# Optimization experiments

Hardware: AMD Instinct MI355X
Metric: run time of the kernel (lower is better)

## Reference

```python
import jax, jax.numpy as jnp
import numpy as np

IMAGE_SIZE = 512


def setup_inputs() -> dict:
    key = jax.random.key(0)
    k1, k2, k3, k4, k5 = jax.random.split(key, 5)
    B, S, C, P = 64, IMAGE_SIZE, 64, IMAGE_SIZE * IMAGE_SIZE
    x = jax.random.normal(k1, (B, S, S), dtype=jnp.float32)
    pattern_importance = jax.random.uniform(k2, (B, C), dtype=jnp.float32)
    idxx = jax.random.randint(k3, (P,), 0, S)
    idxy = jax.random.randint(k4, (P,), 0, S)
    cluster_id = jax.random.randint(k5, (P,), 0, C)
    return {"x": x, "pattern_importance": pattern_importance,
            "idxx": idxx, "idxy": idxy, "cluster_id": cluster_id}


def reference(x, pattern_importance, idxx, idxy, cluster_id):
    S = IMAGE_SIZE
    # fft2 with zero-pad/crop to (S, S), then shift DC to center
    x_fft = jnp.fft.fftshift(jnp.fft.fft2(x, s=(S, S), axes=(-2, -1)), axes=(-2, -1))
    # mask: ones everywhere, per-cluster importance scattered at clustered freq bins
    B = x.shape[0]
    mask = jnp.ones((B, S, S), dtype=x.dtype)
    # mask[j, idxx, idxy] = pattern_importance[j, cluster_id] for all batches j at once
    mask = mask.at[:, idxx, idxy].set(pattern_importance[:, cluster_id])
    x_reject = x_fft * mask
    x_ifft = jnp.real(jnp.fft.ifft2(jnp.fft.ifftshift(x_reject, axes=(-2, -1)),
                                    s=(x.shape[1], x.shape[2]), axes=(-2, -1)))
    return x_ifft
```

## Files before the change

kernel.cpp:

```cpp
#include <hip/hip_runtime.h>

#define INV_N2 (1.0f/262144.0f)
#define RS 264
#define TS 520
#define YH_F2 ((size_t)32768 * RS)

typedef unsigned u32x2 __attribute__((ext_vector_type(2)));

__device__ __forceinline__ int brev9(int v) { return (int)(__brev((unsigned)v) >> 23); }

__device__ __forceinline__ float hsin(float rev) { return __builtin_amdgcn_sinf(rev); }
__device__ __forceinline__ float hcos(float rev) { return __builtin_amdgcn_cosf(rev); }

template<int CTRL>
__device__ __forceinline__ float xdpp(float x) {
  int v = __float_as_int(x);
  return __int_as_float(__builtin_amdgcn_update_dpp(v, v, CTRL, 0xF, 0xF, true));
}
__device__ __forceinline__ float xs1(float x) { return xdpp<0xB1>(x); }
__device__ __forceinline__ float xs2(float x) { return xdpp<0x4E>(x); }
__device__ __forceinline__ float xs8(float x) { return xdpp<0x128>(x); }
__device__ __forceinline__ float xs4(float x) {
  return __int_as_float(__builtin_amdgcn_ds_swizzle(__float_as_int(x), 0x101F));
}
__device__ __forceinline__ float xs16(float x) {
#if __has_builtin(__builtin_amdgcn_permlane16_swap)
  u32x2 r = __builtin_amdgcn_permlane16_swap(__float_as_uint(x), __float_as_uint(x), false, false);
  return __uint_as_float((threadIdx.x & 16) ? r[0] : r[1]);
#else
  return __int_as_float(__builtin_amdgcn_ds_swizzle(__float_as_int(x), 0x401F));
#endif
}
__device__ __forceinline__ float xs32(float x) {
#if __has_builtin(__builtin_amdgcn_permlane32_swap)
  u32x2 r = __builtin_amdgcn_permlane32_swap(__float_as_uint(x), __float_as_uint(x), false, false);
  return __uint_as_float((threadIdx.x & 32) ? r[0] : r[1]);
#else
  return __shfl_xor(x, 32, 64);
#endif
}

__device__ __forceinline__ void bfly_dif(float &ar, float &ai, float &br, float &bi,
                                         float wr, float wi) {
  float sr = ar + br, si = ai + bi;
  float dr = ar - br, di = ai - bi;
  ar = sr; ai = si;
  br = dr*wr - di*wi; bi = dr*wi + di*wr;
}
__device__ __forceinline__ void bfly_dit(float &ar, float &ai, float &br, float &bi,
                                         float wr, float wi) {
  float tr = br*wr - bi*wi, ti = br*wi + bi*wr;
  br = ar - tr; bi = ai - ti;
  ar = ar + tr; ai = ai + ti;
}

#define FWD_XSTAGE(S, XCHG) { \
  const float rev = -(float)(lane & (S-1)) * (0.5f/(float)(S)); \
  float s0 = hsin(rev), c0 = hcos(rev); \
  const bool up = (lane & (S)) != 0; \
  const float sg = up ? -1.0f : 1.0f; \
  const float wr = up ? c0 : 1.0f; \
  const float wi = up ? s0 : 0.0f; \
  _Pragma("unroll") for (int k = 0; k < 8; ++k) { \
    float rr = XCHG(xr[k]); float ri = XCHG(xi[k]); \
    float vr = fmaf(sg, xr[k], rr); float vi = fmaf(sg, xi[k], ri); \
    xr[k] = vr*wr - vi*wi; xi[k] = vr*wi + vi*wr; } }

#define INV_XSTAGE(S, XCHG) { \
  const float rev = (float)(lane & (S-1)) * (0.5f/(float)(S)); \
  float s0 = hsin(rev), c0 = hcos(rev); \
  const bool up = (lane & (S)) != 0; \
  const float wr = up ? c0 : 1.0f; \
  const float wi = up ? s0 : 0.0f; \
  const float sg = up ? -1.0f : 1.0f; \
  _Pragma("unroll") for (int k = 0; k < 8; ++k) { \
    float zr = xr[k]*wr - xi[k]*wi; \
    float zi = xr[k]*wi + xi[k]*wr; \
    float rr = XCHG(zr); float ri = XCHG(zi); \
    xr[k] = fmaf(sg, zr, rr); xi[k] = fmaf(sg, zi, ri); } }

__device__ __forceinline__ void wave_fft512_fwd(float xr[8], float xi[8], int lane) {
  {
    float rev = -(float)lane * (1.0f/512.0f);
    float s0 = hsin(rev), c0 = hcos(rev);
    float wr = c0, wi = s0;
    const float rr8 = 0.70710678118654752f, ri8 = -0.70710678118654752f;
    #pragma unroll
    for (int k = 0; k < 4; ++k) {
      bfly_dif(xr[k], xi[k], xr[k+4], xi[k+4], wr, wi);
      float nr = wr*rr8 - wi*ri8, ni = wr*ri8 + wi*rr8;
      wr = nr; wi = ni;
    }
  }
  {
    float rev = -(float)lane * (1.0f/256.0f);
    float s0 = hsin(rev), c0 = hcos(rev);
    float w0r = c0, w0i = s0;
    float w1r = s0, w1i = -c0;
    bfly_dif(xr[0], xi[0], xr[2], xi[2], w0r, w0i);
    bfly_dif(xr[1], xi[1], xr[3], xi[3], w1r, w1i);
    bfly_dif(xr[4], xi[4], xr[6], xi[6], w0r, w0i);
    bfly_dif(xr[5], xi[5], xr[7], xi[7], w1r, w1i);
  }
  {
    float rev = -(float)lane * (1.0f/128.0f);
    float s0 = hsin(rev), c0 = hcos(rev);
    bfly_dif(xr[0], xi[0], xr[1], xi[1], c0, s0);
    bfly_dif(xr[2], xi[2], xr[3], xi[3], c0, s0);
    bfly_dif(xr[4], xi[4], xr[5], xi[5], c0, s0);
    bfly_dif(xr[6], xi[6], xr[7], xi[7], c0, s0);
  }
  FWD_XSTAGE(32, xs32)
  FWD_XSTAGE(16, xs16)
  FWD_XSTAGE(8,  xs8)
  FWD_XSTAGE(4,  xs4)
  FWD_XSTAGE(2,  xs2)
  {
    const float sg = (lane & 1) ? -1.0f : 1.0f;
    #pragma unroll
    for (int k = 0; k < 8; ++k) {
      float rr = xs1(xr[k]); float ri = xs1(xi[k]);
      xr[k] = fmaf(sg, xr[k], rr); xi[k] = fmaf(sg, xi[k], ri);
    }
  }
}

__device__ __forceinline__ void wave_fft512_inv(float xr[8], float xi[8], int lane) {
  {
    const float sg = (lane & 1) ? -1.0f : 1.0f;
    #pragma unroll
    for (int k = 0; k < 8; ++k) {
      float rr = xs1(xr[k]); float ri = xs1(xi[k]);
      xr[k] = fmaf(sg, xr[k], rr); xi[k] = fmaf(sg, xi[k], ri);
    }
  }
  INV_XSTAGE(2,  xs2)
  INV_XSTAGE(4,  xs4)
  INV_XSTAGE(8,  xs8)
  INV_XSTAGE(16, xs16)
  INV_XSTAGE(32, xs32)
  {
    float rev = (float)lane * (1.0f/128.0f);
    float s0 = hsin(rev), c0 = hcos(rev);
    bfly_dit(xr[0], xi[0], xr[1], xi[1], c0, s0);
    bfly_dit(xr[2], xi[2], xr[3], xi[3], c0, s0);
    bfly_dit(xr[4], xi[4], xr[5], xi[5], c0, s0);
    bfly_dit(xr[6], xi[6], xr[7], xi[7], c0, s0);
  }
  {
    float rev = (float)lane * (1.0f/256.0f);
    float s0 = hsin(rev), c0 = hcos(rev);
    float w0r = c0, w0i = s0;
    float w1r = -s0, w1i = c0;
    bfly_dit(xr[0], xi[0], xr[2], xi[2], w0r, w0i);
    bfly_dit(xr[1], xi[1], xr[3], xi[3], w1r, w1i);
    bfly_dit(xr[4], xi[4], xr[6], xi[6], w0r, w0i);
    bfly_dit(xr[5], xi[5], xr[7], xi[7], w1r, w1i);
  }
  {
    float rev = (float)lane * (1.0f/512.0f);
    float s0 = hsin(rev), c0 = hcos(rev);
    float wr = c0, wi = s0;
    const float rr8 = 0.70710678118654752f, ri8 = 0.70710678118654752f;
    #pragma unroll
    for (int k = 0; k < 4; ++k) {
      bfly_dit(xr[k], xi[k], xr[k+4], xi[k+4], wr, wi);
      float nr = wr*rr8 - wi*ri8, ni = wr*ri8 + wi*rr8;
      wr = nr; wi = ni;
    }
  }
}

__global__ void k_scatter(const int* __restrict__ idxx, const int* __restrict__ idxy,
                          const int* __restrict__ cid, int* __restrict__ W) {
  int p = blockIdx.x * 256 + threadIdx.x;
  int u = (idxx[p] + 256) & 511;
  int v = (idxy[p] + 256) & 511;
  atomicMax(&W[u * 512 + v], (p << 6) | cid[p]);
}

__global__ void k_pack(const int* __restrict__ W, int* __restrict__ pk) {
  int idx = blockIdx.x * 256 + threadIdx.x;
  if (idx >= 264 * 512) return;
  int j = idx >> 9, n = idx & 511;
  int out = (127 << 7) | 127;
  if (j < 257) {
    int v = (j == 256) ? 256 : brev9(2 * j);
    int u = brev9(n);
    int c1 = W[u * 512 + v];
    int c2 = W[((512 - u) & 511) * 512 + ((512 - v) & 511)];
    int a = (c1 < 0) ? 127 : (c1 & 63);
    int b = (c2 < 0) ? 127 : (c2 & 63);
    out = (b << 7) | a;
  }
  pk[j * 512 + n] = out;
}

__global__ __launch_bounds__(512) void k_fwd_rows(const float* __restrict__ x,
                                                  float2* __restrict__ Yh) {
  int w = threadIdx.x >> 6, lane = threadIdx.x & 63;
  int r = blockIdx.x * 8 + w;
  const float* row = x + (size_t)r * 512;
  float xr[8], xi[8];
  #pragma unroll
  for (int k = 0; k < 8; ++k) { xr[k] = row[k*64 + lane]; xi[k] = 0.f; }
  wave_fft512_fwd(xr, xi, lane);
  float2* orow = Yh + (size_t)r * RS;
  if (!(lane & 1)) {
    #pragma unroll
    for (int k = 0; k < 8; ++k) orow[k*32 + (lane >> 1)] = make_float2(xr[k], xi[k]);
  } else if (lane == 1) {
    orow[256] = make_float2(xr[0], xi[0]);
  }
}

__global__ __launch_bounds__(512) void k_cols(float2* __restrict__ Yh,
                                              const int* __restrict__ pk,
                                              const float* __restrict__ pimp) {
  __shared__ float lre[8 * TS], lim[8 * TS];
  __shared__ float pilx[128];
  int tid = threadIdx.x;
  int b = blockIdx.x / 33, g = blockIdx.x % 33;
  float2* base = Yh + (size_t)b * 512 * RS + g * 8;
  #pragma unroll
  for (int rep = 0; rep < 4; ++rep) {
    int m = rep * 512 + tid;
    int i = m >> 2, cp = m & 3;
    float4 v = *(const float4*)(base + (size_t)i * RS + 2 * cp);
    lre[(2*cp)  *TS + i] = v.x; lim[(2*cp)  *TS + i] = v.y;
    lre[(2*cp+1)*TS + i] = v.z; lim[(2*cp+1)*TS + i] = v.w;
  }
  if (tid < 128) pilx[tid] = (tid < 64) ? pimp[b * 64 + tid] : 1.0f;
  __syncthreads();
  int w = tid >> 6, lane = tid & 63;
  float xr[8], xi[8];
  #pragma unroll
  for (int k = 0; k < 8; ++k) {
    xr[k] = lre[w*TS + k*64 + lane];
    xi[k] = lim[w*TS + k*64 + lane];
  }
  wave_fft512_fwd(xr, xi, lane);
  const int* cm = pk + (g * 8 + w) * 512;
  #pragma unroll
  for (int k = 0; k < 8; ++k) {
    int p = cm[k*64 + lane];
    float mm = 0.5f * (pilx[p & 127] + pilx[(p >> 7) & 127]) * INV_N2;
    xr[k] *= mm; xi[k] *= mm;
  }
  wave_fft512_inv(xr, xi, lane);
  #pragma unroll
  for (int k = 0; k < 8; ++k) {
    lre[w*TS + k*64 + lane] = xr[k];
    lim[w*TS + k*64 + lane] = xi[k];
  }
  __syncthreads();
  #pragma unroll
  for (int rep = 0; rep < 4; ++rep) {
    int m = rep * 512 + tid;
    int i = m >> 2, cp = m & 3;
    *(float4*)(base + (size_t)i * RS + 2 * cp) =
      make_float4(lre[(2*cp)*TS + i], lim[(2*cp)*TS + i],
                  lre[(2*cp+1)*TS + i], lim[(2*cp+1)*TS + i]);
  }
}

__global__ __launch_bounds__(512) void k_inv_rows(const float2* __restrict__ Yh,
                                                  float* __restrict__ out) {
  __shared__ float lre[8 * RS], lim[8 * RS];
  int tid = threadIdx.x;
  int w = tid >> 6, lane = tid & 63;
  int r = blockIdx.x * 8 + w;
  const float2* rowp = Yh + (size_t)r * RS;
  #pragma unroll
  for (int k2 = 0; k2 < 5; ++k2) {
    int idx = k2 * 64 + lane;
    if (idx < 257) {
      float2 v = rowp[idx];
      lre[w*RS + idx] = v.x; lim[w*RS + idx] = v.y;
    }
  }
  float xr[8], xi[8];
  #pragma unroll
  for (int k = 0; k < 8; ++k) {
    int n = k * 64 + lane;
    int v9 = brev9(n);
    int j2 = brev9(512 - v9) >> 1;
    int j = (n & 1) ? ((n == 1) ? 256 : j2) : (n >> 1);
    float sgn = ((n & 1) && (n != 1)) ? -1.f : 1.f;
    xr[k] = lre[w*RS + j];
    xi[k] = sgn * lim[w*RS + j];
  }
  wave_fft512_inv(xr, xi, lane);
  float* orow = out + (size_t)r * 512;
  #pragma unroll
  for (int k = 0; k < 8; ++k) orow[k*64 + lane] = xr[k];
}

extern "C" void kernel_launch(void* const* d_in, const int* in_sizes, int n_in,
                              void* d_out, int out_size, void* d_ws, size_t ws_size,
                              hipStream_t stream) {
  const float* x    = (const float*)d_in[0];
  const float* pimp = (const float*)d_in[1];
  const int* idxx   = (const int*)d_in[2];
  const int* idxy   = (const int*)d_in[3];
  const int* cid    = (const int*)d_in[4];

  float2* Yh = (float2*)d_ws;
  int* W  = (int*)((char*)d_ws + YH_F2 * sizeof(float2));
  int* pk = W + 512 * 512;

  hipMemsetAsync(W, 0xFF, 512 * 512 * sizeof(int), stream);
  k_scatter  <<<1024, 256, 0, stream>>>(idxx, idxy, cid, W);
  k_pack     <<<(264 * 512 + 255) / 256, 256, 0, stream>>>(W, pk);
  k_fwd_rows <<<4096, 512, 0, stream>>>(x, Yh);
  k_cols     <<<64 * 33, 512, 0, stream>>>(Yh, pk, pimp);
  k_inv_rows <<<4096, 512, 0, stream>>>(Yh, (float*)d_out);
}
```

Before: 229.2 us.

## Pack two real rows per complex FFT and precompute per-lane twiddles

The row passes now put two real rows into one complex 512-point FFT, with one row as the real part and one as the imaginary part. The two spectra are separated through conjugate symmetry in shared memory, and the inverse pass is recombined the same way, so half as many row blocks are launched. Twiddle sin/cos values are computed once per lane into a struct and reused across the forward and inverse stages instead of being recomputed at every stage. This lowers FFT arithmetic and transcendental work in the row kernels. The cost is extra shared-memory traffic, more registers for the twiddle table, and a risk of bank conflicts from the bit-reversed gather.

```diff
diff --git a/kernel.cpp b/kernel.cpp
--- a/kernel.cpp
+++ b/kernel.cpp
@@ -8,7 +8,6 @@
 typedef unsigned u32x2 __attribute__((ext_vector_type(2)));
 
 __device__ __forceinline__ int brev9(int v) { return (int)(__brev((unsigned)v) >> 23); }
-
 __device__ __forceinline__ float hsin(float rev) { return __builtin_amdgcn_sinf(rev); }
 __device__ __forceinline__ float hcos(float rev) { return __builtin_amdgcn_cosf(rev); }
 
@@ -40,6 +39,24 @@
 #endif
 }
 
+struct Tw { float c[8], s[8]; };
+__device__ __forceinline__ Tw make_tw(int lane) {
+  Tw t;
+  float a0 = (float)lane        * (1.0f/512.0f);
+  float a1 = (float)lane        * (1.0f/256.0f);
+  float a2 = (float)lane        * (1.0f/128.0f);
+  float a3 = (float)(lane & 31) * (1.0f/64.0f);
+  float a4 = (float)(lane & 15) * (1.0f/32.0f);
+  float a5 = (float)(lane & 7)  * (1.0f/16.0f);
+  float a6 = (float)(lane & 3)  * (1.0f/8.0f);
+  float a7 = (float)(lane & 1)  * (1.0f/4.0f);
+  t.c[0]=hcos(a0); t.s[0]=hsin(a0); t.c[1]=hcos(a1); t.s[1]=hsin(a1);
+  t.c[2]=hcos(a2); t.s[2]=hsin(a2); t.c[3]=hcos(a3); t.s[3]=hsin(a3);
+  t.c[4]=hcos(a4); t.s[4]=hsin(a4); t.c[5]=hcos(a5); t.s[5]=hsin(a5);
+  t.c[6]=hcos(a6); t.s[6]=hsin(a6); t.c[7]=hcos(a7); t.s[7]=hsin(a7);
+  return t;
+}
+
 __device__ __forceinline__ void bfly_dif(float &ar, float &ai, float &br, float &bi,
                                          float wr, float wi) {
   float sr = ar + br, si = ai + bi;
@@ -54,24 +71,20 @@
   ar = ar + tr; ai = ai + ti;
 }
 
-#define FWD_XSTAGE(S, XCHG) { \
-  const float rev = -(float)(lane & (S-1)) * (0.5f/(float)(S)); \
-  float s0 = hsin(rev), c0 = hcos(rev); \
+#define FWD_XSTAGE(S, XCHG, CC, SS) { \
   const bool up = (lane & (S)) != 0; \
   const float sg = up ? -1.0f : 1.0f; \
-  const float wr = up ? c0 : 1.0f; \
-  const float wi = up ? s0 : 0.0f; \
+  const float wr = up ? (CC) : 1.0f; \
+  const float wi = up ? -(SS) : 0.0f; \
   _Pragma("unroll") for (int k = 0; k < 8; ++k) { \
     float rr = XCHG(xr[k]); float ri = XCHG(xi[k]); \
     float vr = fmaf(sg, xr[k], rr); float vi = fmaf(sg, xi[k], ri); \
     xr[k] = vr*wr - vi*wi; xi[k] = vr*wi + vi*wr; } }
 
-#define INV_XSTAGE(S, XCHG) { \
-  const float rev = (float)(lane & (S-1)) * (0.5f/(float)(S)); \
-  float s0 = hsin(rev), c0 = hcos(rev); \
+#define INV_XSTAGE(S, XCHG, CC, SS) { \
   const bool up = (lane & (S)) != 0; \
-  const float wr = up ? c0 : 1.0f; \
-  const float wi = up ? s0 : 0.0f; \
+  const float wr = up ? (CC) : 1.0f; \
+  const float wi = up ? (SS) : 0.0f; \
   const float sg = up ? -1.0f : 1.0f; \
   _Pragma("unroll") for (int k = 0; k < 8; ++k) { \
     float zr = xr[k]*wr - xi[k]*wi; \
@@ -79,11 +92,10 @@
     float rr = XCHG(zr); float ri = XCHG(zi); \
     xr[k] = fmaf(sg, zr, rr); xi[k] = fmaf(sg, zi, ri); } }
 
-__device__ __forceinline__ void wave_fft512_fwd(float xr[8], float xi[8], int lane) {
-  {
-    float rev = -(float)lane * (1.0f/512.0f);
-    float s0 = hsin(rev), c0 = hcos(rev);
-    float wr = c0, wi = s0;
+__device__ __forceinline__ void wave_fft512_fwd(float xr[8], float xi[8], int lane,
+                                                const Tw& t) {
+  {
+    float wr = t.c[0], wi = -t.s[0];
     const float rr8 = 0.70710678118654752f, ri8 = -0.70710678118654752f;
     #pragma unroll
     for (int k = 0; k < 4; ++k) {
@@ -93,28 +105,24 @@
     }
   }
   {
-    float rev = -(float)lane * (1.0f/256.0f);
-    float s0 = hsin(rev), c0 = hcos(rev);
-    float w0r = c0, w0i = s0;
-    float w1r = s0, w1i = -c0;
+    float w0r = t.c[1], w0i = -t.s[1];
+    float w1r = -t.s[1], w1i = -t.c[1];
     bfly_dif(xr[0], xi[0], xr[2], xi[2], w0r, w0i);
     bfly_dif(xr[1], xi[1], xr[3], xi[3], w1r, w1i);
     bfly_dif(xr[4], xi[4], xr[6], xi[6], w0r, w0i);
     bfly_dif(xr[5], xi[5], xr[7], xi[7], w1r, w1i);
   }
   {
-    float rev = -(float)lane * (1.0f/128.0f);
-    float s0 = hsin(rev), c0 = hcos(rev);
-    bfly_dif(xr[0], xi[0], xr[1], xi[1], c0, s0);
-    bfly_dif(xr[2], xi[2], xr[3], xi[3], c0, s0);
-    bfly_dif(xr[4], xi[4], xr[5], xi[5], c0, s0);
-    bfly_dif(xr[6], xi[6], xr[7], xi[7], c0, s0);
-  }
-  FWD_XSTAGE(32, xs32)
-  FWD_XSTAGE(16, xs16)
-  FWD_XSTAGE(8,  xs8)
-  FWD_XSTAGE(4,  xs4)
-  FWD_XSTAGE(2,  xs2)
+    bfly_dif(xr[0], xi[0], xr[1], xi[1], t.c[2], -t.s[2]);
+    bfly_dif(xr[2], xi[2], xr[3], xi[3], t.c[2], -t.s[2]);
+    bfly_dif(xr[4], xi[4], xr[5], xi[5], t.c[2], -t.s[2]);
+    bfly_dif(xr[6], xi[6], xr[7], xi[7], t.c[2], -t.s[2]);
+  }
+  FWD_XSTAGE(32, xs32, t.c[3], t.s[3])
+  FWD_XSTAGE(16, xs16, t.c[4], t.s[4])
+  FWD_XSTAGE(8,  xs8,  t.c[5], t.s[5])
+  FWD_XSTAGE(4,  xs4,  t.c[6], t.s[6])
+  FWD_XSTAGE(2,  xs2,  t.c[7], t.s[7])
   {
     const float sg = (lane & 1) ? -1.0f : 1.0f;
     #pragma unroll
@@ -125,7 +133,8 @@
   }
 }
 
-__device__ __forceinline__ void wave_fft512_inv(float xr[8], float xi[8], int lane) {
+__device__ __forceinline__ void wave_fft512_inv(float xr[8], float xi[8], int lane,
+                                                const Tw& t) {
   {
     const float sg = (lane & 1) ? -1.0f : 1.0f;
     #pragma unroll
@@ -134,33 +143,27 @@
       xr[k] = fmaf(sg, xr[k], rr); xi[k] = fmaf(sg, xi[k], ri);
     }
   }
-  INV_XSTAGE(2,  xs2)
-  INV_XSTAGE(4,  xs4)
-  INV_XSTAGE(8,  xs8)
-  INV_XSTAGE(16, xs16)
-  INV_XSTAGE(32, xs32)
-  {
-    float rev = (float)lane * (1.0f/128.0f);
-    float s0 = hsin(rev), c0 = hcos(rev);
-    bfly_dit(xr[0], xi[0], xr[1], xi[1], c0, s0);
-    bfly_dit(xr[2], xi[2], xr[3], xi[3], c0, s0);
-    bfly_dit(xr[4], xi[4], xr[5], xi[5], c0, s0);
-    bfly_dit(xr[6], xi[6], xr[7], xi[7], c0, s0);
-  }
-  {
-    float rev = (float)lane * (1.0f/256.0f);
-    float s0 = hsin(rev), c0 = hcos(rev);
-    float w0r = c0, w0i = s0;
-    float w1r = -s0, w1i = c0;
+  INV_XSTAGE(2,  xs2,  t.c[7], t.s[7])
+  INV_XSTAGE(4,  xs4,  t.c[6], t.s[6])
+  INV_XSTAGE(8,  xs8,  t.c[5], t.s[5])
+  INV_XSTAGE(16, xs16, t.c[4], t.s[4])
+  INV_XSTAGE(32, xs32, t.c[3], t.s[3])
+  {
+    bfly_dit(xr[0], xi[0], xr[1], xi[1], t.c[2], t.s[2]);
+    bfly_dit(xr[2], xi[2], xr[3], xi[3], t.c[2], t.s[2]);
+    bfly_dit(xr[4], xi[4], xr[5], xi[5], t.c[2], t.s[2]);
+    bfly_dit(xr[6], xi[6], xr[7], xi[7], t.c[2], t.s[2]);
+  }
+  {
+    float w0r = t.c[1], w0i = t.s[1];
+    float w1r = -t.s[1], w1i = t.c[1];
     bfly_dit(xr[0], xi[0], xr[2], xi[2], w0r, w0i);
     bfly_dit(xr[1], xi[1], xr[3], xi[3], w1r, w1i);
     bfly_dit(xr[4], xi[4], xr[6], xi[6], w0r, w0i);
     bfly_dit(xr[5], xi[5], xr[7], xi[7], w1r, w1i);
   }
   {
-    float rev = (float)lane * (1.0f/512.0f);
-    float s0 = hsin(rev), c0 = hcos(rev);
-    float wr = c0, wi = s0;
+    float wr = t.c[0], wi = t.s[0];
     const float rr8 = 0.70710678118654752f, ri8 = 0.70710678118654752f;
     #pragma unroll
     for (int k = 0; k < 4; ++k) {
@@ -198,19 +201,36 @@
 
 __global__ __launch_bounds__(512) void k_fwd_rows(const float* __restrict__ x,
                                                   float2* __restrict__ Yh) {
-  int w = threadIdx.x >> 6, lane = threadIdx.x & 63;
-  int r = blockIdx.x * 8 + w;
-  const float* row = x + (size_t)r * 512;
+  __shared__ float zre[8 * 512], zim[8 * 512];
+  int tid = threadIdx.x, w = tid >> 6, lane = tid & 63;
+  int rp = blockIdx.x * 8 + w;
+  const float* rowA = x + (size_t)(2 * rp) * 512;
+  const float* rowB = rowA + 512;
+  Tw t = make_tw(lane);
   float xr[8], xi[8];
   #pragma unroll
-  for (int k = 0; k < 8; ++k) { xr[k] = row[k*64 + lane]; xi[k] = 0.f; }
-  wave_fft512_fwd(xr, xi, lane);
-  float2* orow = Yh + (size_t)r * RS;
-  if (!(lane & 1)) {
-    #pragma unroll
-    for (int k = 0; k < 8; ++k) orow[k*32 + (lane >> 1)] = make_float2(xr[k], xi[k]);
-  } else if (lane == 1) {
-    orow[256] = make_float2(xr[0], xi[0]);
+  for (int k = 0; k < 8; ++k) { xr[k] = rowA[k*64 + lane]; xi[k] = rowB[k*64 + lane]; }
+  wave_fft512_fwd(xr, xi, lane, t);
+  float* zr = zre + w * 512;
+  float* zi = zim + w * 512;
+  #pragma unroll
+  for (int k = 0; k < 8; ++k) { zr[k*64 + lane] = xr[k]; zi[k*64 + lane] = xi[k]; }
+  float2* orowA = Yh + (size_t)(2 * rp) * RS;
+  float2* orowB = orowA + RS;
+  #pragma unroll
+  for (int k = 0; k < 4; ++k) {
+    int j = k * 64 + lane;
+    int n2 = 2 * j;
+    int kf = brev9(n2);
+    int m = brev9((512 - kf) & 511);
+    float er = zr[n2], ei = zi[n2];
+    float mr = zr[m],  mi = zi[m];
+    orowA[j] = make_float2(0.5f * (er + mr), 0.5f * (ei - mi));
+    orowB[j] = make_float2(0.5f * (ei + mi), 0.5f * (mr - er));
+  }
+  if (lane == 0) {
+    orowA[256] = make_float2(zr[1], 0.0f);
+    orowB[256] = make_float2(zi[1], 0.0f);
   }
 }
 
@@ -231,15 +251,17 @@
     lre[(2*cp+1)*TS + i] = v.z; lim[(2*cp+1)*TS + i] = v.w;
   }
   if (tid < 128) pilx[tid] = (tid < 64) ? pimp[b * 64 + tid] : 1.0f;
+  int lane = tid & 63;
+  Tw t = make_tw(lane);
   __syncthreads();
-  int w = tid >> 6, lane = tid & 63;
+  int w = tid >> 6;
   float xr[8], xi[8];
   #pragma unroll
   for (int k = 0; k < 8; ++k) {
     xr[k] = lre[w*TS + k*64 + lane];
     xi[k] = lim[w*TS + k*64 + lane];
   }
-  wave_fft512_fwd(xr, xi, lane);
+  wave_fft512_fwd(xr, xi, lane, t);
   const int* cm = pk + (g * 8 + w) * 512;
   #pragma unroll
   for (int k = 0; k < 8; ++k) {
@@ -247,7 +269,7 @@
     float mm = 0.5f * (pilx[p & 127] + pilx[(p >> 7) & 127]) * INV_N2;
     xr[k] *= mm; xi[k] *= mm;
   }
-  wave_fft512_inv(xr, xi, lane);
+  wave_fft512_inv(xr, xi, lane, t);
   #pragma unroll
   for (int k = 0; k < 8; ++k) {
     lre[w*TS + k*64 + lane] = xr[k];
@@ -266,17 +288,20 @@
 
 __global__ __launch_bounds__(512) void k_inv_rows(const float2* __restrict__ Yh,
                                                   float* __restrict__ out) {
-  __shared__ float lre[8 * RS], lim[8 * RS];
-  int tid = threadIdx.x;
-  int w = tid >> 6, lane = tid & 63;
-  int r = blockIdx.x * 8 + w;
-  const float2* rowp = Yh + (size_t)r * RS;
+  __shared__ float aRe[8*264], aIm[8*264], bRe[8*264], bIm[8*264];
+  int tid = threadIdx.x, w = tid >> 6, lane = tid & 63;
+  int rp = blockIdx.x * 8 + w;
+  const float2* rowA = Yh + (size_t)(2 * rp) * RS;
+  const float2* rowB = rowA + RS;
+  Tw t = make_tw(lane);
+  float* ar_ = aRe + w*264; float* ai_ = aIm + w*264;
+  float* br_ = bRe + w*264; float* bi_ = bIm + w*264;
   #pragma unroll
   for (int k2 = 0; k2 < 5; ++k2) {
     int idx = k2 * 64 + lane;
     if (idx < 257) {
-      float2 v = rowp[idx];
-      lre[w*RS + idx] = v.x; lim[w*RS + idx] = v.y;
+      float2 va = rowA[idx]; ar_[idx] = va.x; ai_[idx] = va.y;
+      float2 vb = rowB[idx]; br_[idx] = vb.x; bi_[idx] = vb.y;
     }
   }
   float xr[8], xi[8];
@@ -284,16 +309,22 @@
   for (int k = 0; k < 8; ++k) {
     int n = k * 64 + lane;
     int v9 = brev9(n);
-    int j2 = brev9(512 - v9) >> 1;
+    int j2 = brev9((512 - v9) & 511) >> 1;
+    bool oddx = (n & 1) && (n != 1);
     int j = (n & 1) ? ((n == 1) ? 256 : j2) : (n >> 1);
-    float sgn = ((n & 1) && (n != 1)) ? -1.f : 1.f;
-    xr[k] = lre[w*RS + j];
-    xi[k] = sgn * lim[w*RS + j];
-  }
-  wave_fft512_inv(xr, xi, lane);
-  float* orow = out + (size_t)r * 512;
-  #pragma unroll
-  for (int k = 0; k < 8; ++k) orow[k*64 + lane] = xr[k];
+    float s = oddx ? -1.0f : 1.0f;
+    float ar = ar_[j], ai = ai_[j], br = br_[j], bi = bi_[j];
+    xr[k] = ar - s * bi;
+    xi[k] = fmaf(s, ai, br);
+  }
+  wave_fft512_inv(xr, xi, lane, t);
+  float* orowA = out + (size_t)(2 * rp) * 512;
+  float* orowB = orowA + 512;
+  #pragma unroll
+  for (int k = 0; k < 8; ++k) {
+    orowA[k*64 + lane] = xr[k];
+    orowB[k*64 + lane] = xi[k];
+  }
 }
 
 extern "C" void kernel_launch(void* const* d_in, const int* in_sizes, int n_in,
@@ -312,7 +343,7 @@
   hipMemsetAsync(W, 0xFF, 512 * 512 * sizeof(int), stream);
   k_scatter  <<<1024, 256, 0, stream>>>(idxx, idxy, cid, W);
   k_pack     <<<(264 * 512 + 255) / 256, 256, 0, stream>>>(W, pk);
-  k_fwd_rows <<<4096, 512, 0, stream>>>(x, Yh);
+  k_fwd_rows <<<2048, 512, 0, stream>>>(x, Yh);
   k_cols     <<<64 * 33, 512, 0, stream>>>(Yh, pk, pimp);
-  k_inv_rows <<<4096, 512, 0, stream>>>(Yh, (float*)d_out);
-}
+  k_inv_rows <<<2048, 512, 0, stream>>>(Yh, (float*)d_out);
+}
```

Measured after the change: 214.0 us. -6.7%, faster.
